# Kernel tuning notes

Hardware: AMD Instinct MI355X
Metric: run time of the kernel (lower is better)

Reference implementation:

```python
import jax, jax.numpy as jnp
import numpy as np
from jax import lax

T, B, F, H, C = 1024, 128, 88, 1024, 88


def setup_inputs() -> dict:
    key = jax.random.key(0)
    ks = jax.random.split(key, 8)
    s = 0.02
    lengths = jnp.sort(jax.random.randint(ks[1], (B,), 1, T + 1))[::-1]  # descending, as pack_padded requires
    return {
        "input_sequences": jax.random.normal(ks[0], (T, B, F), dtype=jnp.float32),
        "input_sequence_lengths": lengths.astype(jnp.int64),
        "W_ih": jax.random.normal(ks[2], (4 * H, F), dtype=jnp.float32) * s,
        "W_hh": jax.random.normal(ks[3], (4 * H, H), dtype=jnp.float32) * s,
        "b_ih": jax.random.normal(ks[4], (4 * H,), dtype=jnp.float32) * s,
        "b_hh": jax.random.normal(ks[5], (4 * H,), dtype=jnp.float32) * s,
        "W_fc": jax.random.normal(ks[6], (C, H), dtype=jnp.float32) * s,
        "b_fc": jax.random.normal(ks[7], (C,), dtype=jnp.float32) * s,
    }


def reference(input_sequences, input_sequence_lengths, W_ih, W_hh, b_ih, b_hh, W_fc, b_fc):
    Tn, Bn, _ = input_sequences.shape
    Hn = W_hh.shape[1]
    # mask[t, b] = True iff timestep t is within sequence b (equivalent to :batch_size_t slicing
    # when lengths are sorted descending, as the torch code assumes)
    mask_seq = jnp.arange(Tn)[:, None] < input_sequence_lengths[None, :]  # [T, B]

    h0 = jnp.zeros((Bn, Hn), dtype=input_sequences.dtype)
    c0 = jnp.zeros((Bn, Hn), dtype=input_sequences.dtype)

    def step(carry, inp):
        h, c = carry
        x, m = inp  # x: [B, F], m: [B]
        gates = x @ W_ih.T + b_ih + h @ W_hh.T + b_hh  # [B, 4H], order i,f,g,o
        i, f, g, o = jnp.split(gates, 4, axis=1)
        c_new = jax.nn.sigmoid(f) * c + jax.nn.sigmoid(i) * jnp.tanh(g)
        h_new = jax.nn.sigmoid(o) * jnp.tanh(c_new)
        mb = m[:, None]
        h2 = jnp.where(mb, h_new, h)
        c2 = jnp.where(mb, c_new, c)
        logits_t = jnp.where(mb, h2 @ W_fc.T + b_fc, 0.0)  # rows beyond batch_size_t stay zero
        return (h2, c2), logits_t

    (_, _), predictions = lax.scan(step, (h0, c0), (input_sequences, mask_seq))  # [T, B, C]

    logits = jnp.transpose(predictions, (1, 0, 2))  # [B, T, C]
    binary_logits = jnp.stack((logits, 1.0 - logits), axis=3)  # [B, T, C, 2]
    return binary_logits.reshape(-1, 2)
```

## Files before the change

### kernel.cpp

```cpp
#include <hip/hip_runtime.h>
#include <cstdint>
#include <cstddef>

#define T_STEPS 1024
#define B_SZ    128
#define F_SZ    88
#define H_SZ    1024
#define C_SZ    88

#define N_GATE_WG 128
#define N_FC_WG   6
#define N_COMPUTE (N_GATE_WG + N_FC_WG)
#define N_WG      N_COMPUTE
#define BLOCK     128
#define FLAG_STRIDE 16
#define RING      16

typedef __attribute__((ext_vector_type(8)))  __bf16 bf16x8;
typedef __attribute__((ext_vector_type(16))) float  f32x16;
typedef __attribute__((ext_vector_type(4)))  int    i32x4;

#define SLAB_OFF    0
#define SLAB_BYTES  (64 * 1024 * 2)
#define BIAS_OFF    (SLAB_OFF + SLAB_BYTES)
#define LENL_OFF    (BIAS_OFF + 256)
#define NB_OFF      (LENL_OFF + 512)
#define EXCH_OFF    (NB_OFF + 2064)
#define EXCH_WAVE   (32 * 68 * 4)
#define STAGE_OFF   (EXCH_OFF + 2 * EXCH_WAVE)
#define SMEM_BYTES  (STAGE_OFF + 2 * 512 * 2)

#define HBUF_ELEMS  131072
#define HBUF_BYTES  (HBUF_ELEMS * 2)

__device__ __forceinline__ float sigm(float x) {
    return __builtin_amdgcn_rcpf(1.0f + __expf(-x));
}
__device__ __forceinline__ float tanh_fast(float x) {
    return 1.0f - 2.0f * __builtin_amdgcn_rcpf(__expf(2.0f * x) + 1.0f);
}
__device__ __forceinline__ void st_llc(void* p, uint64_t v) {
    __hip_atomic_store((uint64_t*)p, v, __ATOMIC_RELAXED,
                       __HIP_MEMORY_SCOPE_AGENT);
}

extern "C" __global__ void __launch_bounds__(BLOCK, 1)
lstm_fused(const float* __restrict__ X,
           const int*   __restrict__ len_raw,
           const float* __restrict__ W_ih,
           const float* __restrict__ W_hh,
           const float* __restrict__ b_ih,
           const float* __restrict__ b_hh,
           const float* __restrict__ W_fc,
           const float* __restrict__ b_fc,
           float*       __restrict__ out,
           __bf16*      __restrict__ hbuf,
           int*         __restrict__ flags)
{
    extern __shared__ char smem[];
    __bf16*         slab  = (__bf16*)(smem + SLAB_OFF);
    float*          biasL = (float*)(smem + BIAS_OFF);
    int*            lenL  = (int*)(smem + LENL_OFF);
    unsigned short* nbL   = (unsigned short*)(smem + NB_OFF);

    const int  wg   = blockIdx.x;
    const int  tid  = threadIdx.x;
    const int  w    = tid >> 6;
    const int  lane = tid & 63;
    const int  col  = lane & 31;
    const int  h5   = lane >> 5;
    const bool isGate = (wg < N_GATE_WG);

    int ug = 0, bt2 = 0, cg = 0;
    if (isGate) { int m = wg >> 3, x = wg & 7; bt2 = x >> 2; ug = 4 * m + (x & 3); }
    else        { int f = wg - N_GATE_WG; bt2 = f / 3; cg = f % 3; }
    const int bti  = bt2 * 2 + w;
    const int fidx = bt2 * 68 + (isGate ? ug : (64 + cg));
    const int hbase = bt2 * 68;

    const int lstride = (len_raw[1] == 0) ? 2 : 1;
    if (tid < B_SZ) lenL[tid] = len_raw[tid * lstride];
    __syncthreads();
    for (int t = tid; t <= T_STEPS; t += BLOCK) {
        int cnt = 0;
        #pragma unroll 4
        for (int b = 0; b < B_SZ; ++b) cnt += (lenL[b] > t) ? 1 : 0;
        nbL[t] = (unsigned short)cnt;
    }

    bf16x8 wih[2][6];
    if (isGate) {
        for (int idx = tid; idx < 64 * 1024; idx += BLOCK) {
            int cc2 = idx >> 10, k = idx & 1023;
            int n = cc2 >> 5, cc = cc2 & 31;
            int gate = cc & 3, ul = cc >> 2;
            int j = ug * 16 + n * 8 + ul;
            float v = W_hh[(size_t)(gate * H_SZ + j) * H_SZ + k];
            slab[(size_t)((k >> 4) * 128 + n * 64 + ((k >> 3) & 1) * 32 + cc) * 8 + (k & 7)] = (__bf16)v;
        }
        {
            const int gate = col & 3, ul = col >> 2;
            #pragma unroll
            for (int n = 0; n < 2; ++n) {
                const float* wrow = W_ih + (size_t)(gate * H_SZ + ug * 16 + n * 8 + ul) * F_SZ;
                #pragma unroll
                for (int kt = 0; kt < 6; ++kt) {
                    const int f0 = kt * 16 + h5 * 8;
                    bf16x8 b;
                    #pragma unroll
                    for (int e = 0; e < 8; ++e) {
                        int k = f0 + e;
                        b[e] = (k < F_SZ) ? (__bf16)wrow[k] : (__bf16)0.0f;
                    }
                    wih[n][kt] = b;
                }
            }
        }
        if (tid < 64) {
            int n = tid >> 5, cc = tid & 31, gate = cc & 3, ul = cc >> 2;
            int row = gate * H_SZ + ug * 16 + n * 8 + ul;
            biasL[tid] = b_ih[row] + b_hh[row];
        }
    } else {
        for (int idx = tid; idx < 32 * 1024; idx += BLOCK) {
            int cc = idx >> 10, k = idx & 1023;
            int c = cg * 32 + cc;
            float v = (c < C_SZ) ? W_fc[(size_t)c * H_SZ + k] : 0.0f;
            slab[(size_t)((k >> 4) * 64 + ((k >> 3) & 1) * 32 + cc) * 8 + (k & 7)] = (__bf16)v;
        }
        if (tid < 32) {
            int c = cg * 32 + tid;
            biasL[tid] = (c < C_SZ) ? b_fc[c] : 0.0f;
        }
    }

    __syncthreads();
    if (tid == 0) {
        __builtin_amdgcn_s_waitcnt(0);
        __hip_atomic_store(flags + fidx * FLAG_STRIDE, 1, __ATOMIC_RELAXED,
                           __HIP_MEMORY_SCOPE_AGENT);
    }

    const int a4    = col & 3;
    const int u0    = col >> 2;
    const int c0fc  = cg * 32;
    const int phase = wg & (RING - 1);

    float*  exch   = (float*)(smem + EXCH_OFF) + w * (EXCH_WAVE / 4);
    __bf16* stageW = (__bf16*)(smem + STAGE_OFF) + w * 512;

    const bool hasFC = (lane < 3);
    long guard = 0;

    float c_reg[8] = {0.f,0.f,0.f,0.f,0.f,0.f,0.f,0.f};
    float h_reg[8] = {0.f,0.f,0.f,0.f,0.f,0.f,0.f,0.f};

    for (int t = 0; t <= T_STEPS; ++t) {
        const int nb_t   = (t < T_STEPS) ? (int)nbL[t] : 0;
        const int nb_pre = (t > 0) ? (int)nbL[t - 1] : B_SZ;
        const __bf16* hin  = hbuf + (size_t)((t + RING - 1) & (RING - 1)) * HBUF_ELEMS;
        __bf16*       hout = hbuf + (size_t)(t & (RING - 1)) * HBUF_ELEMS;

        const bool gcomp = isGate && (t < T_STEPS) && (bti * 32 < nb_t);
        const bool gwrt  = isGate && (t < T_STEPS) && (bti * 32 < nb_pre);

        f32x16 acc[2];

        if (gcomp) {
            #pragma unroll
            for (int n = 0; n < 2; ++n) {
                float bv = biasL[n * 32 + col];
                #pragma unroll
                for (int i = 0; i < 16; ++i) acc[n][i] = bv;
            }
            const float* xrow = X + ((size_t)t * B_SZ + (bti * 32 + col)) * F_SZ;
            #pragma unroll
            for (int kt = 0; kt < 6; ++kt) {
                int f0 = kt * 16 + h5 * 8;
                bf16x8 a;
                if (f0 < F_SZ) {
                    float4 lo = *(const float4*)(xrow + f0);
                    float4 hi = *(const float4*)(xrow + f0 + 4);
                    a[0] = (__bf16)lo.x; a[1] = (__bf16)lo.y; a[2] = (__bf16)lo.z; a[3] = (__bf16)lo.w;
                    a[4] = (__bf16)hi.x; a[5] = (__bf16)hi.y; a[6] = (__bf16)hi.z; a[7] = (__bf16)hi.w;
                } else {
                    #pragma unroll
                    for (int j = 0; j < 8; ++j) a[j] = (__bf16)0.0f;
                }
                #pragma unroll
                for (int n = 0; n < 2; ++n)
                    acc[n] = __builtin_amdgcn_mfma_f32_32x32x16_bf16(a, wih[n][kt], acc[n], 0, 0, 0);
            }
        }

        if (w == 0) {
            const int target = t + 1;
            for (;;) {
                int a = __hip_atomic_load(flags + (hbase + lane) * FLAG_STRIDE,
                                          __ATOMIC_RELAXED, __HIP_MEMORY_SCOPE_AGENT);
                int b = hasFC ? __hip_atomic_load(flags + (hbase + 64 + lane) * FLAG_STRIDE,
                                                  __ATOMIC_RELAXED, __HIP_MEMORY_SCOPE_AGENT)
                              : target;
                if (__all((a >= target) && (b >= target))) break;
                __builtin_amdgcn_s_sleep(1);
                if (++guard > 400000000L) break;
            }
        }
        __syncthreads();

        if (((t + phase) & (RING - 1)) == 0) {
            if (tid == 0)
                __builtin_amdgcn_fence(__ATOMIC_ACQUIRE, "agent");
            __syncthreads();
        }

        if (!isGate && tid == 0) {
            __hip_atomic_store(flags + fidx * FLAG_STRIDE, t + 2, __ATOMIC_RELAXED,
                               __HIP_MEMORY_SCOPE_AGENT);
        }

        if (!isGate && t >= 1) {
            const int  s        = t - 1;
            const int  nb_s     = (int)nbL[s];
            const bool act_tile = (bti * 32) < nb_s;
            f32x16 accf;
            #pragma unroll
            for (int i = 0; i < 16; ++i) accf[i] = 0.0f;
            if (act_tile) {
                float bv = biasL[col];
                #pragma unroll
                for (int i = 0; i < 16; ++i) accf[i] = bv;
                const __bf16* hA = hin + (size_t)bti * 512 + (size_t)lane * 8;
                const __bf16* bB = slab + lane * 8;
                #pragma unroll 8
                for (int kt = 0; kt < 64; ++kt) {
                    bf16x8 a = __builtin_bit_cast(bf16x8, *(const i32x4*)(hA + (size_t)kt * 2048));
                    bf16x8 b = __builtin_bit_cast(bf16x8, *(const i32x4*)(bB + (size_t)kt * 512));
                    accf = __builtin_amdgcn_mfma_f32_32x32x16_bf16(a, b, accf, 0, 0, 0);
                }
            }
            const int c = c0fc + col;
            if (c < C_SZ) {
                #pragma unroll
                for (int i = 0; i < 16; ++i) {
                    int row = (i & 3) + 8 * (i >> 2) + 4 * h5;
                    int b   = bti * 32 + row;
                    float v = (act_tile && b < nb_s) ? accf[i] : 0.0f;
                    float2 o2; o2.x = v; o2.y = 1.0f - v;
                    *(float2*)(out + ((size_t)(b * T_STEPS + s) * C_SZ + c) * 2) = o2;
                }
            }
        }

        if (gcomp && t > 0) {
            const __bf16* hA = hin + (size_t)bti * 512 + (size_t)lane * 8;
            const __bf16* bB = slab + lane * 8;
            i32x4 pf0[16], pf1[16];
            #pragma unroll
            for (int i = 0; i < 16; ++i)
                pf0[i] = *(const i32x4*)(hA + (size_t)i * 2048);
            #pragma unroll
            for (int i = 0; i < 16; ++i)
                pf1[i] = *(const i32x4*)(hA + (size_t)(16 + i) * 2048);
            __builtin_amdgcn_sched_barrier(0);
            #pragma unroll
            for (int c = 0; c < 4; ++c) {
                i32x4 (&cur)[16] = (c & 1) ? pf1 : pf0;
                #pragma unroll
                for (int i = 0; i < 16; ++i) {
                    bf16x8 a = __builtin_bit_cast(bf16x8, cur[i]);
                    const int ks = c * 16 + i;
                    bf16x8 b0 = __builtin_bit_cast(bf16x8,
                        *(const i32x4*)(bB + (size_t)ks * 1024));
                    acc[0] = __builtin_amdgcn_mfma_f32_32x32x16_bf16(a, b0, acc[0], 0, 0, 0);
                    bf16x8 b1 = __builtin_bit_cast(bf16x8,
                        *(const i32x4*)(bB + (size_t)ks * 1024 + 512));
                    acc[1] = __builtin_amdgcn_mfma_f32_32x32x16_bf16(a, b1, acc[1], 0, 0, 0);
                    if (c < 2)
                        cur[i] = *(const i32x4*)(hA + (size_t)((c + 2) * 16 + i) * 2048);
                }
                __builtin_amdgcn_sched_barrier(0);
            }
        }
        if (gcomp) {
            #pragma unroll
            for (int n = 0; n < 2; ++n)
                #pragma unroll
                for (int j = 0; j < 16; ++j)
                    exch[(n * 16 + j) * 68 + lane] = acc[n][j];
        }
        __syncthreads();

        if (gcomp) {
            #pragma unroll
            for (int n = 0; n < 2; ++n) {
                #pragma unroll
                for (int q = 0; q < 4; ++q) {
                    const float4 v = *(const float4*)(exch + (n * 16 + 4 * a4 + q) * 68 + 32 * h5 + (col & ~3));
                    float si = sigm(v.x);
                    float sf = sigm(v.y);
                    float tg = tanh_fast(v.z);
                    float so = sigm(v.w);
                    float cn = sf * c_reg[n * 4 + q] + si * tg;
                    float hn = so * tanh_fast(cn);
                    int b = bti * 32 + 8 * a4 + 4 * h5 + q;
                    if (b < nb_t) { c_reg[n * 4 + q] = cn; h_reg[n * 4 + q] = hn; }
                }
            }
        }
        if (gwrt) {
            #pragma unroll
            for (int n = 0; n < 2; ++n)
                #pragma unroll
                for (int q = 0; q < 4; ++q)
                    stageW[(8 * a4 + 4 * h5 + q) * 16 + n * 8 + u0] = (__bf16)h_reg[n * 4 + q];
        }
        __syncthreads();

        if (gwrt) {
            const uint64_t* sp = (const uint64_t*)(stageW + (size_t)col * 16 + (size_t)h5 * 8);
            uint64_t* hp = (uint64_t*)(hout + (size_t)ug * 2048 + (size_t)bti * 512 + (size_t)lane * 8);
            st_llc(hp,     sp[0]);
            st_llc(hp + 1, sp[1]);
        }
        __syncthreads();

        if (isGate && tid == 0) {
            __builtin_amdgcn_s_waitcnt(0);
            __hip_atomic_store(flags + fidx * FLAG_STRIDE, t + 2, __ATOMIC_RELAXED,
                               __HIP_MEMORY_SCOPE_AGENT);
        }
    }
}

extern "C" void kernel_launch(void* const* d_in, const int* in_sizes, int n_in,
                              void* d_out, int out_size, void* d_ws, size_t ws_size,
                              hipStream_t stream) {
    const float* X    = (const float*)d_in[0];
    const int*   lens = (const int*)d_in[1];
    const float* Wih  = (const float*)d_in[2];
    const float* Whh  = (const float*)d_in[3];
    const float* bih  = (const float*)d_in[4];
    const float* bhh  = (const float*)d_in[5];
    const float* Wfc  = (const float*)d_in[6];
    const float* bfc  = (const float*)d_in[7];
    float*       outp = (float*)d_out;

    __bf16* hbuf  = (__bf16*)d_ws;
    int*    flags = (int*)((char*)d_ws + (size_t)RING * HBUF_BYTES);

    (void)hipFuncSetAttribute((const void*)lstm_fused,
                              hipFuncAttributeMaxDynamicSharedMemorySize, SMEM_BYTES);

    void* args[] = { (void*)&X, (void*)&lens, (void*)&Wih, (void*)&Whh,
                     (void*)&bih, (void*)&bhh, (void*)&Wfc, (void*)&bfc,
                     (void*)&outp, (void*)&hbuf, (void*)&flags };
    hipError_t le = hipLaunchCooperativeKernel((void*)lstm_fused, dim3(N_WG), dim3(BLOCK),
                                               args, (unsigned)SMEM_BYTES, stream);
    if (le != hipSuccess) {
        hipLaunchKernelGGL(lstm_fused, dim3(N_WG), dim3(BLOCK),
                           (unsigned)SMEM_BYTES, stream,
                           X, lens, Wih, Whh, bih, bhh, Wfc, bfc, outp, hbuf, flags);
    }
}
```

Baseline: 7.562 ms.

## Make cross-workgroup flag sync per-wave instead of per-workgroup

Each wave now owns its own progress flag, indexed by batch tile instead of workgroup pair, and polls only the flags of the producers it depends on. All __syncthreads barriers in the timestep loop are removed, and LDS exchange and staging are ordered by per-wave lgkmcnt waits instead. This is meant to cut the intra-workgroup barrier cost and let the two waves of a workgroup progress independently across timesteps. It doubles the flag count and the polling traffic, and it relies on each wave's LDS region being private so the exchange stays correct without a barrier.

Measured after the change: 7.502 ms. About the same (-0.8%).

```diff
diff --git a/kernel.cpp b/kernel.cpp
--- a/kernel.cpp
+++ b/kernel.cpp
@@ -75,8 +75,8 @@
     if (isGate) { int m = wg >> 3, x = wg & 7; bt2 = x >> 2; ug = 4 * m + (x & 3); }
     else        { int f = wg - N_GATE_WG; bt2 = f / 3; cg = f % 3; }
     const int bti  = bt2 * 2 + w;
-    const int fidx = bt2 * 68 + (isGate ? ug : (64 + cg));
-    const int hbase = bt2 * 68;
+    const int fidx  = bti * 68 + (isGate ? ug : (64 + cg));
+    const int gbase = bti * 68;
 
     const int lstride = (len_raw[1] == 0) ? 2 : 1;
     if (tid < B_SZ) lenL[tid] = len_raw[tid * lstride];
@@ -135,11 +135,10 @@
     }
 
     __syncthreads();
-    if (tid == 0) {
-        __builtin_amdgcn_s_waitcnt(0);
+    __builtin_amdgcn_s_waitcnt(0);
+    if (lane == 0)
         __hip_atomic_store(flags + fidx * FLAG_STRIDE, 1, __ATOMIC_RELAXED,
                            __HIP_MEMORY_SCOPE_AGENT);
-    }
 
     const int a4    = col & 3;
     const int u0    = col >> 2;
@@ -149,7 +148,6 @@
     float*  exch   = (float*)(smem + EXCH_OFF) + w * (EXCH_WAVE / 4);
     __bf16* stageW = (__bf16*)(smem + STAGE_OFF) + w * 512;
 
-    const bool hasFC = (lane < 3);
     long guard = 0;
 
     float c_reg[8] = {0.f,0.f,0.f,0.f,0.f,0.f,0.f,0.f};
@@ -193,28 +191,25 @@
             }
         }
 
-        if (w == 0) {
+        {
             const int target = t + 1;
             for (;;) {
-                int a = __hip_atomic_load(flags + (hbase + lane) * FLAG_STRIDE,
+                int a = __hip_atomic_load(flags + (gbase + lane) * FLAG_STRIDE,
                                           __ATOMIC_RELAXED, __HIP_MEMORY_SCOPE_AGENT);
-                int b = hasFC ? __hip_atomic_load(flags + (hbase + 64 + lane) * FLAG_STRIDE,
-                                                  __ATOMIC_RELAXED, __HIP_MEMORY_SCOPE_AGENT)
-                              : target;
+                int b = (lane < 3) ? __hip_atomic_load(flags + (gbase + 64 + lane) * FLAG_STRIDE,
+                                                       __ATOMIC_RELAXED, __HIP_MEMORY_SCOPE_AGENT)
+                                   : target;
                 if (__all((a >= target) && (b >= target))) break;
                 __builtin_amdgcn_s_sleep(1);
                 if (++guard > 400000000L) break;
             }
-        }
-        __syncthreads();
-
-        if (((t + phase) & (RING - 1)) == 0) {
-            if (tid == 0)
-                __builtin_amdgcn_fence(__ATOMIC_ACQUIRE, "agent");
-            __syncthreads();
-        }
-
-        if (!isGate && tid == 0) {
+            asm volatile("" ::: "memory");
+        }
+
+        if (((t + phase) & (RING - 1)) == 0)
+            __builtin_amdgcn_fence(__ATOMIC_ACQUIRE, "agent");
+
+        if (!isGate && lane == 0) {
             __hip_atomic_store(flags + fidx * FLAG_STRIDE, t + 2, __ATOMIC_RELAXED,
                                __HIP_MEMORY_SCOPE_AGENT);
         }
@@ -282,16 +277,15 @@
                 __builtin_amdgcn_sched_barrier(0);
             }
         }
+
         if (gcomp) {
             #pragma unroll
             for (int n = 0; n < 2; ++n)
                 #pragma unroll
                 for (int j = 0; j < 16; ++j)
                     exch[(n * 16 + j) * 68 + lane] = acc[n][j];
-        }
-        __syncthreads();
-
-        if (gcomp) {
+            asm volatile("s_waitcnt lgkmcnt(0)" ::: "memory");
+            __builtin_amdgcn_sched_barrier(0);
             #pragma unroll
             for (int n = 0; n < 2; ++n) {
                 #pragma unroll
@@ -308,27 +302,27 @@
                 }
             }
         }
+
         if (gwrt) {
             #pragma unroll
             for (int n = 0; n < 2; ++n)
                 #pragma unroll
                 for (int q = 0; q < 4; ++q)
                     stageW[(8 * a4 + 4 * h5 + q) * 16 + n * 8 + u0] = (__bf16)h_reg[n * 4 + q];
-        }
-        __syncthreads();
-
-        if (gwrt) {
+            asm volatile("s_waitcnt lgkmcnt(0)" ::: "memory");
+            __builtin_amdgcn_sched_barrier(0);
             const uint64_t* sp = (const uint64_t*)(stageW + (size_t)col * 16 + (size_t)h5 * 8);
             uint64_t* hp = (uint64_t*)(hout + (size_t)ug * 2048 + (size_t)bti * 512 + (size_t)lane * 8);
             st_llc(hp,     sp[0]);
             st_llc(hp + 1, sp[1]);
         }
-        __syncthreads();
-
-        if (isGate && tid == 0) {
+
+        if (isGate) {
+            asm volatile("" ::: "memory");
             __builtin_amdgcn_s_waitcnt(0);
-            __hip_atomic_store(flags + fidx * FLAG_STRIDE, t + 2, __ATOMIC_RELAXED,
-                               __HIP_MEMORY_SCOPE_AGENT);
+            if (lane == 0)
+                __hip_atomic_store(flags + fidx * FLAG_STRIDE, t + 2, __ATOMIC_RELAXED,
+                                   __HIP_MEMORY_SCOPE_AGENT);
         }
     }
 }
```
